# Kernel tuning notes

Hardware: AMD Instinct MI355X
Metric: run time of the kernel (lower is better)

Reference implementation:

```python
import jax, jax.numpy as jnp
import numpy as np

B, S, D = 2, 2048, 1024
H = 16
DH = D // H  # 64


def setup_inputs() -> dict:
    key = jax.random.key(0)
    k1, k2, k3 = jax.random.split(key, 3)
    X = jax.random.normal(k1, (B, S, D), dtype=jnp.float32)
    # xavier_normal for Linear(D, 3*D): std = sqrt(2/(fan_in+fan_out))
    std_qkv = float(np.sqrt(2.0 / (D + 3 * D)))
    std_out = float(np.sqrt(2.0 / (D + D)))
    W_qkv = jax.random.normal(k2, (3 * H * DH, D), dtype=jnp.float32) * std_qkv
    W_out = jax.random.normal(k3, (D, H * DH), dtype=jnp.float32) * std_out
    return {"X": X, "W_qkv": W_qkv, "W_out": W_out}


def reference(X, W_qkv, W_out):
    b, s, d = X.shape
    # stacked projection: (b, s, 3*H*DH), then per-head chunk into q,k,v
    qkv = jnp.einsum('bsd,ed->bse', X, W_qkv)
    qkv = qkv.reshape(b, s, H, 3 * DH)
    q, k, v = jnp.split(qkv, 3, axis=-1)  # each (b, s, H, DH)
    scale = 1.0 / jnp.sqrt(jnp.asarray(DH, dtype=X.dtype))
    # naive unfused attention: full [b,H,s,s] score matrix
    scores = jnp.einsum('bqhd,bkhd->bhqk', q, k) * scale
    attn = jax.nn.softmax(scores, axis=-1)
    vals = jnp.einsum('bhqk,bkhd->bqhd', attn, v)
    vals = vals.reshape(b, s, H * DH)
    out = jnp.einsum('bse,de->bsd', vals, W_out)
    return out
```

## Files before the change

kernel.cpp:

```cpp
#include <hip/hip_runtime.h>
#include <cstdint>
#include <cstddef>

typedef __bf16 bf16;
typedef __bf16 bf16x8 __attribute__((ext_vector_type(8)));
typedef __bf16 bf16x2 __attribute__((ext_vector_type(2)));
typedef float  floatx4 __attribute__((ext_vector_type(4)));
typedef unsigned uintx4 __attribute__((ext_vector_type(4)));

typedef __attribute__((address_space(1))) void gvoid_t;
typedef __attribute__((address_space(3))) void lvoid_t;

#define MFMA16(a, b, c) __builtin_amdgcn_mfma_f32_16x16x32_bf16((a), (b), (c), 0, 0, 0)

#if __has_builtin(__builtin_amdgcn_exp2f)
#define EXP2(x) __builtin_amdgcn_exp2f(x)
#else
#define EXP2(x) exp2f(x)
#endif

#define S_TOK 2048
#define E3 3072
#define DMODEL 1024

#define NX 4194304
#define NWQ 3145728
#define NWO 1048576
__global__ __launch_bounds__(256) void cvt_all(const float* __restrict__ X,
                                               const float* __restrict__ Wq,
                                               const float* __restrict__ Wo,
                                               bf16* __restrict__ Xb,
                                               bf16* __restrict__ Wqb,
                                               bf16* __restrict__ Wob) {
  int i = (blockIdx.x * 256 + threadIdx.x) * 8;
  const float* s;
  bf16* d;
  float sc = 1.0f;
  int off;
  if (i < NX) {
    s = X; d = Xb; off = i;
  } else if (i < NX + NWQ) {
    off = i - NX; s = Wq; d = Wqb;
    int row = off >> 10;
    if ((row % 192) < 64) sc = 0.18033688011f;
  } else {
    off = i - NX - NWQ; s = Wo; d = Wob;
  }
  const float4* p = (const float4*)(s + off);
  float4 a = p[0], b = p[1];
  bf16x8 o;
  o[0] = (bf16)(a.x * sc); o[1] = (bf16)(a.y * sc);
  o[2] = (bf16)(a.z * sc); o[3] = (bf16)(a.w * sc);
  o[4] = (bf16)(b.x * sc); o[5] = (bf16)(b.y * sc);
  o[6] = (bf16)(b.z * sc); o[7] = (bf16)(b.w * sc);
  *(bf16x8*)(d + off) = o;
}

__device__ __forceinline__ void gl_lds16(const bf16* g, bf16* l) {
  __builtin_amdgcn_global_load_lds((gvoid_t*)g, (lvoid_t*)l, 16, 0, 0);
}

template <bool OUT_BF16, bool FUSE_V>
__global__ __launch_bounds__(256) void gemm_bt(const bf16* __restrict__ A,
                                               const bf16* __restrict__ Bt,
                                               void* __restrict__ Cv,
                                               bf16* __restrict__ Vt,
                                               int M, int N, int K) {
  __shared__ bf16 sA[128 * 64];
  __shared__ bf16 sB[128 * 64];
  const int tid = threadIdx.x;
  const int wv = tid >> 6, lane = tid & 63;
  const int wr = wv >> 1, wc = wv & 1;
  const int lrow = lane & 15, lgrp = lane >> 4;
  const int R0 = blockIdx.y * 128, C0 = blockIdx.x * 128;

  floatx4 acc[4][4] = {};

  const int srow = lane >> 3;
  const int schk = (lane & 7) ^ srow;
  const bf16* gA = A + (size_t)(R0 + wv * 32 + srow) * K + schk * 8;
  const bf16* gB = Bt + (size_t)(C0 + wv * 32 + srow) * K + schk * 8;
  bf16* lA = sA + wv * 32 * 64;
  bf16* lB = sB + wv * 32 * 64;
  const size_t rs8 = (size_t)8 * K;

  for (int k0 = 0; k0 < K; k0 += 64) {
#pragma unroll
    for (int c = 0; c < 4; c++) {
      gl_lds16(gA + k0 + c * rs8, lA + c * 512);
      gl_lds16(gB + k0 + c * rs8, lB + c * 512);
    }
    __syncthreads();
#pragma unroll
    for (int kk = 0; kk < 2; kk++) {
      bf16x8 af[4], bfr[4];
#pragma unroll
      for (int i = 0; i < 4; i++) {
        int r = wr * 64 + i * 16 + lrow;
        af[i] = *(const bf16x8*)&sA[r * 64 + ((kk * 4 + lgrp) ^ (r & 7)) * 8];
      }
#pragma unroll
      for (int j = 0; j < 4; j++) {
        int r = wc * 64 + j * 16 + lrow;
        bfr[j] = *(const bf16x8*)&sB[r * 64 + ((kk * 4 + lgrp) ^ (r & 7)) * 8];
      }
#pragma unroll
      for (int i = 0; i < 4; i++)
#pragma unroll
        for (int j = 0; j < 4; j++)
          acc[i][j] = MFMA16(af[i], bfr[j], acc[i][j]);
    }
    __syncthreads();
  }

  const int rbase = R0 + wr * 64 + lgrp * 4;
  const int cbase = C0 + wc * 64 + lrow;
  if (OUT_BF16) {
    bf16* C = (bf16*)Cv;
#pragma unroll
    for (int i = 0; i < 4; i++)
#pragma unroll
      for (int j = 0; j < 4; j++) {
        const int col = cbase + j * 16;
        const int m192 = col % 192;
        const int hh = col / 192;
#pragma unroll
        for (int r = 0; r < 4; r++) {
          const int row = rbase + i * 16 + r;
          bf16 val = (bf16)acc[i][j][r];
          bf16* dst;
          if (FUSE_V && m192 >= 128) {
            const int sl = row & 2047;
            const int sl5 = sl & 31;
            const int q5 = (((sl5 >> 2) & 3) << 3) | (((sl5 >> 4) & 1) << 2) | (sl5 & 3);
            const int sp = (sl & ~31) | q5;
            dst = Vt + ((size_t)(((row >> 11) * 16 + hh) * 64 + (m192 - 128))) * S_TOK + sp;
          } else {
            dst = C + (size_t)row * N + col;
          }
          *dst = val;
        }
      }
  } else {
    float* C = (float*)Cv;
#pragma unroll
    for (int i = 0; i < 4; i++)
#pragma unroll
      for (int j = 0; j < 4; j++)
#pragma unroll
        for (int r = 0; r < 4; r++)
          C[(size_t)(rbase + i * 16 + r) * N + cbase + j * 16] = acc[i][j][r];
  }
}

__global__ __launch_bounds__(256) void gemm_bt_n64(const bf16* __restrict__ A,
                                                   const bf16* __restrict__ Bt,
                                                   float* __restrict__ C,
                                                   int M, int N, int K) {
  __shared__ bf16 sA[128 * 64];
  __shared__ bf16 sB[64 * 64];
  const int tid = threadIdx.x;
  const int wv = tid >> 6, lane = tid & 63;
  const int wr = wv >> 1, wc = wv & 1;
  const int lrow = lane & 15, lgrp = lane >> 4;
  const int R0 = blockIdx.y * 128, C0 = blockIdx.x * 64;

  floatx4 acc[4][2] = {};

  const int srow = lane >> 3;
  const int schk = (lane & 7) ^ srow;
  const bf16* gA = A + (size_t)(R0 + wv * 32 + srow) * K + schk * 8;
  const bf16* gB = Bt + (size_t)(C0 + wv * 16 + srow) * K + schk * 8;
  bf16* lA = sA + wv * 32 * 64;
  bf16* lB = sB + wv * 16 * 64;
  const size_t rs8 = (size_t)8 * K;

  for (int k0 = 0; k0 < K; k0 += 64) {
#pragma unroll
    for (int c = 0; c < 4; c++) gl_lds16(gA + k0 + c * rs8, lA + c * 512);
#pragma unroll
    for (int c = 0; c < 2; c++) gl_lds16(gB + k0 + c * rs8, lB + c * 512);
    __syncthreads();
#pragma unroll
    for (int kk = 0; kk < 2; kk++) {
      bf16x8 af[4], bfr[2];
#pragma unroll
      for (int i = 0; i < 4; i++) {
        int r = wr * 64 + i * 16 + lrow;
        af[i] = *(const bf16x8*)&sA[r * 64 + ((kk * 4 + lgrp) ^ (r & 7)) * 8];
      }
#pragma unroll
      for (int j = 0; j < 2; j++) {
        int r = wc * 32 + j * 16 + lrow;
        bfr[j] = *(const bf16x8*)&sB[r * 64 + ((kk * 4 + lgrp) ^ (r & 7)) * 8];
      }
#pragma unroll
      for (int i = 0; i < 4; i++)
#pragma unroll
        for (int j = 0; j < 2; j++)
          acc[i][j] = MFMA16(af[i], bfr[j], acc[i][j]);
    }
    __syncthreads();
  }

  const int rbase = R0 + wr * 64 + lgrp * 4;
  const int cbase = C0 + wc * 32 + lrow;
#pragma unroll
  for (int i = 0; i < 4; i++)
#pragma unroll
    for (int j = 0; j < 2; j++)
#pragma unroll
      for (int r = 0; r < 4; r++)
        C[(size_t)(rbase + i * 16 + r) * N + cbase + j * 16] = acc[i][j][r];
}

__global__ __launch_bounds__(512, 4) void attn(const bf16* __restrict__ qkv,
                                               const bf16* __restrict__ Vt,
                                               bf16* __restrict__ vals) {
  __shared__ bf16 sK[2][128 * 64];
  __shared__ bf16 sV[2][64 * 128];

  const int tid = threadIdx.x;
  const int wv = tid >> 6, lane = tid & 63;
  const int lrow = lane & 15, lgrp = lane >> 4;
  const int b = blockIdx.z, h = blockIdx.x;
  const int qb = blockIdx.y * 128;

  const int srow = lane >> 3;
  const int scol = (lane & 7) ^ srow;
  const bf16* kg0 = qkv + (size_t)(b * S_TOK + wv * 8 + srow) * E3 + h * 192 + 64 + scol * 8;
  const int vrow = lane >> 4;
  const int vchk = lane & 15;
  const int d0 = wv * 8 + vrow, d1 = d0 + 4;
  const bf16* vg0 = Vt + (size_t)((b * 16 + h) * 64 + d0) * S_TOK + (vchk ^ (d0 & 15)) * 8;
  const bf16* vg1 = Vt + (size_t)((b * 16 + h) * 64 + d1) * S_TOK + (vchk ^ (d1 & 15)) * 8;

  const bf16* qp = qkv + (size_t)(b * S_TOK + qb + wv * 16) * E3 + h * 192;
  bf16x8 qa[2];
#pragma unroll
  for (int dh = 0; dh < 2; dh++)
    qa[dh] = *(const bf16x8*)(qp + (size_t)lrow * E3 + dh * 32 + lgrp * 8);

  floatx4 O[4] = {};
  float lsum = 0.f;

  auto stage = [&](int buf, int st) {
    const bf16* kg = kg0 + (size_t)st * 128 * E3;
    gl_lds16(kg, &sK[buf][wv * 512]);
    gl_lds16(kg + (size_t)64 * E3, &sK[buf][4096 + wv * 512]);
    gl_lds16(vg0 + st * 128, &sV[buf][wv * 1024]);
    gl_lds16(vg1 + st * 128, &sV[buf][wv * 1024 + 512]);
  };

  auto qk_g = [&](int buf, int g, floatx4 (&sc)[2]) {
    bf16x8 kf[2][2];
#pragma unroll
    for (int t = 0; t < 2; t++)
#pragma unroll
      for (int dh = 0; dh < 2; dh++)
        kf[t][dh] = *(const bf16x8*)&sK[buf][(g * 32 + t * 16 + lrow) * 64 +
                                            ((dh * 4 + lgrp) ^ (lrow & 7)) * 8];
    __builtin_amdgcn_s_setprio(1);
    floatx4 a0 = {0.f, 0.f, 0.f, 0.f}, a1 = {0.f, 0.f, 0.f, 0.f};
    a0 = MFMA16(kf[0][0], qa[0], a0);
    a0 = MFMA16(kf[0][1], qa[1], a0);
    a1 = MFMA16(kf[1][0], qa[0], a1);
    a1 = MFMA16(kf[1][1], qa[1], a1);
    sc[0] = a0;
    sc[1] = a1;
    __builtin_amdgcn_s_setprio(0);
  };

  auto sm_g = [&](floatx4 (&sc)[2], unsigned (&pfw)[4]) {
    float e0 = EXP2(sc[0][0]), e1 = EXP2(sc[0][1]);
    float e2 = EXP2(sc[0][2]), e3 = EXP2(sc[0][3]);
    float e4 = EXP2(sc[1][0]), e5 = EXP2(sc[1][1]);
    float e6 = EXP2(sc[1][2]), e7 = EXP2(sc[1][3]);
    lsum += ((e0 + e1) + (e2 + e3)) + ((e4 + e5) + (e6 + e7));
    bf16x2 w;
    w[0] = (bf16)e0; w[1] = (bf16)e1;
    pfw[0] = __builtin_bit_cast(unsigned, w);
    w[0] = (bf16)e2; w[1] = (bf16)e3;
    pfw[1] = __builtin_bit_cast(unsigned, w);
    w[0] = (bf16)e4; w[1] = (bf16)e5;
    pfw[2] = __builtin_bit_cast(unsigned, w);
    w[0] = (bf16)e6; w[1] = (bf16)e7;
    pfw[3] = __builtin_bit_cast(unsigned, w);
  };

  auto pv_g = [&](int buf, int g, unsigned (&pfw)[4]) {
    bf16x8 vf[4];
#pragma unroll
    for (int dt = 0; dt < 4; dt++)
      vf[dt] = *(const bf16x8*)&sV[buf][(dt * 16 + lrow) * 128 + ((g * 4 + lgrp) ^ lrow) * 8];
    __builtin_amdgcn_s_setprio(1);
    uintx4 pw = {pfw[0], pfw[1], pfw[2], pfw[3]};
    bf16x8 pf = __builtin_bit_cast(bf16x8, pw);
#pragma unroll
    for (int dt = 0; dt < 4; dt++) O[dt] = MFMA16(pf, vf[dt], O[dt]);
    __builtin_amdgcn_s_setprio(0);
  };

  auto compute = [&](int buf) {
    floatx4 scA[2], scB[2];
    unsigned pfA[4], pfB[4];
    qk_g(buf, 0, scA); sm_g(scA, pfA);
    qk_g(buf, 1, scB); sm_g(scB, pfB); pv_g(buf, 0, pfA);
    qk_g(buf, 2, scA); sm_g(scA, pfA); pv_g(buf, 1, pfB);
    qk_g(buf, 3, scB); sm_g(scB, pfB); pv_g(buf, 2, pfA);
    pv_g(buf, 3, pfB);
  };

  stage(0, 0);
  __syncthreads();
#pragma unroll 1
  for (int st = 0; st < 16; st += 2) {
    stage(1, st + 1);
    compute(0);
    __syncthreads();
    if (st + 2 < 16) stage(0, st + 2);
    compute(1);
    __syncthreads();
  }

  lsum += __shfl_xor(lsum, 16);
  lsum += __shfl_xor(lsum, 32);

  bf16* vout = vals + (size_t)(b * S_TOK + qb + wv * 16) * DMODEL + h * 64;
#pragma unroll
  for (int r = 0; r < 4; r++) {
    float rs = __shfl(lsum, lgrp * 4 + r);
    float rinv = __builtin_amdgcn_rcpf(rs);
#pragma unroll
    for (int dt = 0; dt < 4; dt++)
      vout[(size_t)(lgrp * 4 + r) * DMODEL + dt * 16 + lrow] =
          (bf16)(O[dt][r] * rinv);
  }
}

extern "C" void kernel_launch(void* const* d_in, const int* in_sizes, int n_in,
                              void* d_out, int out_size, void* d_ws, size_t ws_size,
                              hipStream_t stream) {
  const float* X = (const float*)d_in[0];
  const float* Wqkv = (const float*)d_in[1];
  const float* Wout = (const float*)d_in[2];
  float* out = (float*)d_out;

  char* ws = (char*)d_ws;
  bf16* Xb = (bf16*)(ws);
  bf16* Wqb = (bf16*)(ws + ((size_t)8 << 20));
  bf16* Wob = (bf16*)(ws + ((size_t)14 << 20));
  bf16* qkvb = (bf16*)(ws + ((size_t)16 << 20));
  bf16* Vt = (bf16*)(ws + ((size_t)40 << 20));
  bf16* vals = (bf16*)(ws + ((size_t)48 << 20));

  cvt_all<<<(NX + NWQ + NWO) / 2048, 256, 0, stream>>>(X, Wqkv, Wout, Xb, Wqb, Wob);

  gemm_bt<true, true><<<dim3(24, 32), 256, 0, stream>>>(Xb, Wqb, qkvb, Vt, 4096, 3072, 1024);

  attn<<<dim3(16, 16, 2), 512, 0, stream>>>(qkvb, Vt, vals);

  gemm_bt_n64<<<dim3(16, 32), 256, 0, stream>>>(vals, Wob, out, 4096, 1024, 1024);
}
```

Measured before the change: 172.2 us.

## Write Q transposed and K head-contiguous from QKV GEMM epilogue with vector stores

The QKV GEMM epilogue now scatters Q into a per-head transposed buffer and K into a per-head contiguous [token,64] buffer, and writes Q and V with 4-wide bf16 vector stores instead of scalar stores. The attention kernel reads K tiles from a contiguous head-major layout (stride 64 instead of 3072) and gathers Q fragments from the transposed buffer. This aims to improve coalescing and locality of K loads in attention and to cut epilogue store count. In exchange, the Q fragment load becomes eight strided scalar reads per fragment, and the K epilogue still uses strided scalar stores.

```diff
diff --git a/kernel.cpp b/kernel.cpp
--- a/kernel.cpp
+++ b/kernel.cpp
@@ -4,6 +4,7 @@
 
 typedef __bf16 bf16;
 typedef __bf16 bf16x8 __attribute__((ext_vector_type(8)));
+typedef __bf16 bf16x4 __attribute__((ext_vector_type(4)));
 typedef __bf16 bf16x2 __attribute__((ext_vector_type(2)));
 typedef float  floatx4 __attribute__((ext_vector_type(4)));
 typedef unsigned uintx4 __attribute__((ext_vector_type(4)));
@@ -65,6 +66,7 @@
                                                const bf16* __restrict__ Bt,
                                                void* __restrict__ Cv,
                                                bf16* __restrict__ Vt,
+                                               bf16* __restrict__ Qt,
                                                int M, int N, int K) {
   __shared__ bf16 sA[128 * 64];
   __shared__ bf16 sB[128 * 64];
@@ -116,31 +118,50 @@
   const int rbase = R0 + wr * 64 + lgrp * 4;
   const int cbase = C0 + wc * 64 + lrow;
   if (OUT_BF16) {
-    bf16* C = (bf16*)Cv;
-#pragma unroll
-    for (int i = 0; i < 4; i++)
-#pragma unroll
-      for (int j = 0; j < 4; j++) {
-        const int col = cbase + j * 16;
-        const int m192 = col % 192;
-        const int hh = col / 192;
-#pragma unroll
-        for (int r = 0; r < 4; r++) {
-          const int row = rbase + i * 16 + r;
-          bf16 val = (bf16)acc[i][j][r];
-          bf16* dst;
-          if (FUSE_V && m192 >= 128) {
-            const int sl = row & 2047;
-            const int sl5 = sl & 31;
-            const int q5 = (((sl5 >> 2) & 3) << 3) | (((sl5 >> 4) & 1) << 2) | (sl5 & 3);
-            const int sp = (sl & ~31) | q5;
-            dst = Vt + ((size_t)(((row >> 11) * 16 + hh) * 64 + (m192 - 128))) * S_TOK + sp;
-          } else {
-            dst = C + (size_t)row * N + col;
-          }
-          *dst = val;
+    const int bb = R0 >> 11;
+    const int tokb0 = rbase & 2047;
+#pragma unroll
+    for (int j = 0; j < 4; j++) {
+      const int col = cbase + j * 16;
+      const int m192 = col % 192;
+      const int hh = col / 192;
+      if (FUSE_V && m192 < 64) {
+        bf16* qdst = Qt + (size_t)((bb * 16 + hh) * 64 + m192) * S_TOK + tokb0;
+#pragma unroll
+        for (int i = 0; i < 4; i++) {
+          bf16x4 v;
+          v[0] = (bf16)acc[i][j][0]; v[1] = (bf16)acc[i][j][1];
+          v[2] = (bf16)acc[i][j][2]; v[3] = (bf16)acc[i][j][3];
+          *(bf16x4*)(qdst + i * 16) = v;
         }
-      }
+      } else if (FUSE_V && m192 >= 128) {
+        bf16* vdst = Vt + (size_t)((bb * 16 + hh) * 64 + (m192 - 128)) * S_TOK;
+#pragma unroll
+        for (int i = 0; i < 4; i++) {
+          const int t0 = tokb0 + i * 16;
+          const int b5 = t0 & 31;
+          const int q5 = (((b5 >> 2) & 3) << 3) | (((b5 >> 4) & 1) << 2);
+          bf16x4 v;
+          v[0] = (bf16)acc[i][j][0]; v[1] = (bf16)acc[i][j][1];
+          v[2] = (bf16)acc[i][j][2]; v[3] = (bf16)acc[i][j][3];
+          *(bf16x4*)(vdst + ((t0 & ~31) | q5)) = v;
+        }
+      } else if (FUSE_V) {
+        bf16* kdst = (bf16*)Cv + ((size_t)((bb * 16 + hh) * 2048 + tokb0)) * 64 + (m192 - 64);
+#pragma unroll
+        for (int i = 0; i < 4; i++)
+#pragma unroll
+          for (int r = 0; r < 4; r++)
+            kdst[(size_t)(i * 16 + r) * 64] = (bf16)acc[i][j][r];
+      } else {
+        bf16* C = (bf16*)Cv;
+#pragma unroll
+        for (int i = 0; i < 4; i++)
+#pragma unroll
+          for (int r = 0; r < 4; r++)
+            C[(size_t)(rbase + i * 16 + r) * N + col] = (bf16)acc[i][j][r];
+      }
+    }
   } else {
     float* C = (float*)Cv;
 #pragma unroll
@@ -214,8 +235,9 @@
         C[(size_t)(rbase + i * 16 + r) * N + cbase + j * 16] = acc[i][j][r];
 }
 
-__global__ __launch_bounds__(512, 4) void attn(const bf16* __restrict__ qkv,
+__global__ __launch_bounds__(512, 4) void attn(const bf16* __restrict__ Kc,
                                                const bf16* __restrict__ Vt,
+                                               const bf16* __restrict__ Qt,
                                                bf16* __restrict__ vals) {
   __shared__ bf16 sK[2][128 * 64];
   __shared__ bf16 sV[2][64 * 128];
@@ -228,26 +250,28 @@
 
   const int srow = lane >> 3;
   const int scol = (lane & 7) ^ srow;
-  const bf16* kg0 = qkv + (size_t)(b * S_TOK + wv * 8 + srow) * E3 + h * 192 + 64 + scol * 8;
+  const bf16* kg0 = Kc + (size_t)((b * 16 + h) * 2048 + wv * 8 + srow) * 64 + scol * 8;
   const int vrow = lane >> 4;
   const int vchk = lane & 15;
   const int d0 = wv * 8 + vrow, d1 = d0 + 4;
   const bf16* vg0 = Vt + (size_t)((b * 16 + h) * 64 + d0) * S_TOK + (vchk ^ (d0 & 15)) * 8;
   const bf16* vg1 = Vt + (size_t)((b * 16 + h) * 64 + d1) * S_TOK + (vchk ^ (d1 & 15)) * 8;
 
-  const bf16* qp = qkv + (size_t)(b * S_TOK + qb + wv * 16) * E3 + h * 192;
+  const bf16* qtp = Qt + (size_t)((b * 16 + h) * 64) * S_TOK + (qb + wv * 16 + lrow);
   bf16x8 qa[2];
 #pragma unroll
   for (int dh = 0; dh < 2; dh++)
-    qa[dh] = *(const bf16x8*)(qp + (size_t)lrow * E3 + dh * 32 + lgrp * 8);
+#pragma unroll
+    for (int j = 0; j < 8; j++)
+      qa[dh][j] = qtp[(size_t)(dh * 32 + lgrp * 8 + j) * S_TOK];
 
   floatx4 O[4] = {};
   float lsum = 0.f;
 
   auto stage = [&](int buf, int st) {
-    const bf16* kg = kg0 + (size_t)st * 128 * E3;
+    const bf16* kg = kg0 + (size_t)st * 128 * 64;
     gl_lds16(kg, &sK[buf][wv * 512]);
-    gl_lds16(kg + (size_t)64 * E3, &sK[buf][4096 + wv * 512]);
+    gl_lds16(kg + 64 * 64, &sK[buf][4096 + wv * 512]);
     gl_lds16(vg0 + st * 128, &sV[buf][wv * 1024]);
     gl_lds16(vg1 + st * 128, &sV[buf][wv * 1024 + 512]);
   };
@@ -350,15 +374,16 @@
   bf16* Xb = (bf16*)(ws);
   bf16* Wqb = (bf16*)(ws + ((size_t)8 << 20));
   bf16* Wob = (bf16*)(ws + ((size_t)14 << 20));
-  bf16* qkvb = (bf16*)(ws + ((size_t)16 << 20));
-  bf16* Vt = (bf16*)(ws + ((size_t)40 << 20));
-  bf16* vals = (bf16*)(ws + ((size_t)48 << 20));
+  bf16* Kc = (bf16*)(ws + ((size_t)16 << 20));
+  bf16* Vt = (bf16*)(ws + ((size_t)24 << 20));
+  bf16* Qt = (bf16*)(ws + ((size_t)32 << 20));
+  bf16* vals = (bf16*)(ws + ((size_t)40 << 20));
 
   cvt_all<<<(NX + NWQ + NWO) / 2048, 256, 0, stream>>>(X, Wqkv, Wout, Xb, Wqb, Wob);
 
-  gemm_bt<true, true><<<dim3(24, 32), 256, 0, stream>>>(Xb, Wqb, qkvb, Vt, 4096, 3072, 1024);
-
-  attn<<<dim3(16, 16, 2), 512, 0, stream>>>(qkvb, Vt, vals);
+  gemm_bt<true, true><<<dim3(24, 32), 256, 0, stream>>>(Xb, Wqb, Kc, Vt, Qt, 4096, 3072, 1024);
+
+  attn<<<dim3(16, 16, 2), 512, 0, stream>>>(Kc, Vt, Qt, vals);
 
   gemm_bt_n64<<<dim3(16, 32), 256, 0, stream>>>(vals, Wob, out, 4096, 1024, 1024);
 }
```

Measured after the change: 167.2 us (median of 2 runs). 1.03x faster.
